# Performance work log

Hardware: AMD Instinct MI355X
Metric: run time of the kernel (lower is better)

Reference implementation:

```python
import jax, jax.numpy as jnp
import numpy as np

B, H, W, C = 32, 128, 128, 64
MX, MY = 32, 32  # modes_x, modes_y


def setup_inputs() -> dict:
    key = jax.random.key(0)
    k1, k2, k3, k4 = jax.random.split(key, 4)
    # glorot-ish scales for the spectral and conv weights
    wscale = (2.0 / (C + C)) ** 0.5
    return {
        "x": jax.random.normal(k1, (B, H, W, C), dtype=jnp.float32),
        "w_real": jax.random.normal(k2, (MX, MY, C, C), dtype=jnp.float32) * wscale,
        "w_imag": jax.random.normal(k3, (MX, MY, C, C), dtype=jnp.float32) * wscale,
        "conv_w": jax.random.normal(k4, (C, C), dtype=jnp.float32) * wscale,
        "conv_b": jnp.zeros((C,), dtype=jnp.float32),
    }


def reference(x, w_real, w_imag, conv_w, conv_b):
    # Complex spectral mixing weights [MX, MY, Cin, Cout]
    weights = jax.lax.complex(w_real, w_imag)
    # tf.signal.fft2d transforms the innermost TWO axes of [B,H,W,C],
    # i.e. axes (W, C); jnp.fft.fft2 default axes=(-2,-1) matches exactly.
    x_ft = jnp.fft.fft2(x.astype(jnp.complex64))           # [B,H,W,C] complex64
    # Mode truncation on axes (H, W), as in the original code.
    x_ft_trunc = x_ft[:, :MX, :MY, :]                      # [B,MX,MY,C]
    # Complex channel-mixing einsum over the low modes.
    x_ft_proc = jnp.einsum('bxyi,xyio->bxyo', x_ft_trunc, weights)  # [B,MX,MY,C]
    # Zero-pad back to the full grid on (H, W).
    x_ft_padded = jnp.pad(x_ft_proc,
                          ((0, 0), (0, H - MX), (0, W - MY), (0, 0)))
    # IFFT again over innermost two axes (W, C), take real part.
    x_spec = jnp.real(jnp.fft.ifft2(x_ft_padded))          # [B,H,W,C] float32
    # 1x1 conv (pointwise channel mix) + bias on the raw input.
    x_local = jnp.einsum('bhwi,io->bhwo', x, conv_w) + conv_b
    return jax.nn.relu(x_spec + x_local)
```

## Files before the change

kernel.cpp:

```cpp
#include <hip/hip_runtime.h>

typedef __attribute__((ext_vector_type(8))) short short8;
typedef __attribute__((ext_vector_type(4))) short bf16x4;
typedef __attribute__((ext_vector_type(4))) float f32x4;
typedef unsigned short ushort_t;

#define MFMA(a, b, c) __builtin_amdgcn_mfma_f32_16x16x32_bf16((a), (b), (c), 0, 0, 0)

constexpr int NB = 32, NHt = 128, NWd = 128, NC = 64, MX = 32;
constexpr float TWO_PI = 6.28318530717958647692f;

constexpr size_t TAB_T1 = 0;
constexpr size_t TAB_T2 = 16384;
constexpr size_t TAB_T3 = 32768;
constexpr size_t TAB_T4 = 49152;
constexpr size_t XY_OFF = 65536;

__device__ inline ushort_t f2bf(float f) {
    union { float f; unsigned int u; } v; v.f = f;
    unsigned int r = v.u + 0x7FFFu + ((v.u >> 16) & 1u);
    return (ushort_t)(r >> 16);
}
__device__ inline int sxor(int row) { return ((row >> 3) & 3) << 4; }

__global__ __launch_bounds__(256) void k0_tables(ushort_t* __restrict__ tabs)
{
    int e = blockIdx.x * 256 + threadIdx.x;
    int tab = e >> 9, rem = e & 511;
    float re[8], im[8];
    if (tab == 0) {
        int mt = rem >> 8, ks = (rem >> 6) & 3, l = rem & 63;
        int uu = (l & 15) + 16 * mt, wb = (l >> 4) * 8 + 32 * ks;
        #pragma unroll
        for (int j = 0; j < 8; ++j) {
            float a = (float)((uu * (wb + j)) & 127) * (TWO_PI / 128.f);
            re[j] = cosf(a); im[j] = -sinf(a);
        }
    } else if (tab == 1) {
        int nt = rem >> 7, ks = (rem >> 6) & 1, l = rem & 63;
        int kk = (l & 15) + 16 * nt, cb2 = (l >> 4) * 8 + 32 * ks;
        #pragma unroll
        for (int j = 0; j < 8; ++j) {
            float a = (float)((kk * (cb2 + j)) & 63) * (TWO_PI / 64.f);
            re[j] = cosf(a); im[j] = -sinf(a);
        }
    } else if (tab == 2) {
        int nt = rem >> 7, ks = (rem >> 6) & 1, l = rem & 63;
        int cc = (l & 15) + 16 * nt, ob = (l >> 4) * 8 + 32 * ks;
        #pragma unroll
        for (int j = 0; j < 8; ++j) {
            float a = (float)(((ob + j) * cc) & 63) * (TWO_PI / 64.f);
            re[j] = cosf(a); im[j] = sinf(a);
        }
    } else {
        int mt = rem >> 6, l = rem & 63;
        int w = (l & 15) + 16 * mt, ub = (l >> 4) * 8;
        #pragma unroll
        for (int j = 0; j < 8; ++j) {
            float a = (float)((w * (ub + j)) & 127) * (TWO_PI / 128.f);
            re[j] = cosf(a) * 0.0001220703125f;
            im[j] = sinf(a) * 0.0001220703125f;
        }
    }
    ushort_t* dst = tabs + (size_t)e * 16;
    #pragma unroll
    for (int j = 0; j < 8; ++j) { dst[j] = f2bf(re[j]); dst[8 + j] = f2bf(im[j]); }
}

__global__ __launch_bounds__(512) void k1_fwd(
    const float* __restrict__ x, const char* __restrict__ tabs, ushort_t* __restrict__ XY)
{
    const int b = blockIdx.x, h = blockIdx.y;
    const int tid = threadIdx.x, lane = tid & 63, wv = tid >> 6;
    constexpr int SXT  = 0;
    constexpr int M1RE = 17408;
    constexpr int M1IM = 17408 + 4608;
    __shared__ __align__(16) char sm[26624];

    const float* xs = x + ((size_t)(b * NHt + h)) * (NWd * NC);
    #pragma unroll
    for (int i = 0; i < 4; ++i) {
        int idx = tid + 512 * i;
        int w = idx >> 4, c4 = (idx & 15) * 4;
        f32x4 v = *reinterpret_cast<const f32x4*>(xs + w * 64 + c4);
        #pragma unroll
        for (int j = 0; j < 4; ++j)
            *(ushort_t*)(sm + SXT + (c4 + j) * 272 + ((w * 2) ^ sxor(c4 + j))) = f2bf(v[j]);
    }
    __syncthreads();

    const int mt = wv >> 2, nt = wv & 3;
    f32x4 m1r = {0.f,0.f,0.f,0.f}, m1i = {0.f,0.f,0.f,0.f};
    const int cc = (lane & 15) + 16 * nt;
    #pragma unroll
    for (int ks = 0; ks < 4; ++ks) {
        short8 bfrag = *reinterpret_cast<const short8*>(
            sm + SXT + cc * 272 + (((lane >> 4) * 16 + 64 * ks) ^ sxor(cc)));
        const char* t1 = tabs + TAB_T1 + (((mt * 4 + ks) * 64 + lane) * 32);
        short8 are = *reinterpret_cast<const short8*>(t1);
        short8 aim = *reinterpret_cast<const short8*>(t1 + 16);
        m1r = MFMA(are, bfrag, m1r);
        m1i = MFMA(aim, bfrag, m1i);
    }
    #pragma unroll
    for (int r = 0; r < 4; ++r) {
        int u = (lane >> 4) * 4 + r + 16 * mt;
        int c = (lane & 15) + 16 * nt;
        *(ushort_t*)(sm + M1RE + u * 144 + c * 2) = f2bf(m1r[r]);
        *(ushort_t*)(sm + M1IM + u * 144 + c * 2) = f2bf(m1i[r]);
    }
    __syncthreads();

    f32x4 xP = {0.f,0.f,0.f,0.f}, xQ = {0.f,0.f,0.f,0.f}, xI = {0.f,0.f,0.f,0.f};
    #pragma unroll
    for (int ks = 0; ks < 2; ++ks) {
        short8 are = *reinterpret_cast<const short8*>(
            sm + M1RE + ((lane & 15) + 16 * mt) * 144 + (lane >> 4) * 16 + 64 * ks);
        short8 aim = *reinterpret_cast<const short8*>(
            sm + M1IM + ((lane & 15) + 16 * mt) * 144 + (lane >> 4) * 16 + 64 * ks);
        const char* t2 = tabs + TAB_T2 + (((nt * 2 + ks) * 64 + lane) * 32);
        short8 bre = *reinterpret_cast<const short8*>(t2);
        short8 bim = *reinterpret_cast<const short8*>(t2 + 16);
        xP = MFMA(are, bre, xP);
        xQ = MFMA(aim, bim, xQ);
        xI = MFMA(are, bim, xI);
        xI = MFMA(aim, bre, xI);
    }
    #pragma unroll
    for (int r = 0; r < 4; ++r) {
        int u = (lane >> 4) * 4 + r + 16 * mt;
        int k = (lane & 15) + 16 * nt;
        *(ushort_t*)(sm + SXT + 0    + u * 128 + k * 2) = f2bf(xP[r] - xQ[r]);
        *(ushort_t*)(sm + SXT + 4096 + u * 128 + k * 2) = f2bf(xI[r]);
    }
    __syncthreads();

    {
        int u = tid >> 4, comp = (tid >> 3) & 1, k8 = (tid & 7) * 8;
        short8 v = *reinterpret_cast<const short8*>(sm + SXT + comp * 4096 + u * 128 + k8 * 2);
        size_t hu = (size_t)(h * 32 + u);
        *reinterpret_cast<short8*>(XY + ((hu * 2 + comp) * 32 + b) * 64 + k8) = v;
    }
}

__global__ __launch_bounds__(256) void k2_mix(
    const float* __restrict__ wre, const float* __restrict__ wim, ushort_t* __restrict__ XY)
{
    const int h = blockIdx.x, u = blockIdx.y;
    const int tid = threadIdx.x, lane = tid & 63, wv = tid >> 6;
    constexpr int XRE = 0, XIM = 4608, WTR = 9216, WTI = 18432;
    __shared__ __align__(16) char sm[27648];
    const size_t hu = (size_t)(h * 32 + u);

    #pragma unroll
    for (int it = 0; it < 2; ++it) {
        int row = (tid >> 3) + 32 * it;
        int comp = row >> 5, bb = row & 31, k8 = (tid & 7) * 8;
        short8 v = *reinterpret_cast<const short8*>(XY + ((hu * 2 + comp) * 32 + bb) * 64 + k8);
        *reinterpret_cast<short8*>(sm + (comp ? XIM : XRE) + bb * 144 + k8 * 2) = v;
    }
    const float* wr = wre + hu * 4096;
    const float* wi = wim + hu * 4096;
    #pragma unroll
    for (int i = 0; i < 4; ++i) {
        int idx = tid + 256 * i;
        int k = idx >> 4, o4 = (idx & 15) * 4;
        f32x4 vr = __builtin_nontemporal_load(reinterpret_cast<const f32x4*>(wr + k * 64 + o4));
        f32x4 vi = __builtin_nontemporal_load(reinterpret_cast<const f32x4*>(wi + k * 64 + o4));
        #pragma unroll
        for (int j = 0; j < 4; ++j) {
            int o = o4 + j, koff = (k * 2) ^ sxor(o);
            *(ushort_t*)(sm + WTR + o * 144 + koff) = f2bf(vr[j]);
            *(ushort_t*)(sm + WTI + o * 144 + koff) = f2bf(vi[j]);
        }
    }
    __syncthreads();

    const int mt = wv >> 1;
    f32x4 yRe[2], yIm[2];
    #pragma unroll
    for (int half = 0; half < 2; ++half) {
        const int nt = (wv & 1) * 2 + half;
        const int oo = (lane & 15) + 16 * nt;
        f32x4 yP = {0.f,0.f,0.f,0.f}, yQ = {0.f,0.f,0.f,0.f}, yI = {0.f,0.f,0.f,0.f};
        #pragma unroll
        for (int ks = 0; ks < 2; ++ks) {
            int woff = ((lane >> 4) * 16 + 64 * ks) ^ sxor(oo);
            short8 are = *reinterpret_cast<const short8*>(
                sm + XRE + ((lane & 15) + 16 * mt) * 144 + (lane >> 4) * 16 + 64 * ks);
            short8 aim = *reinterpret_cast<const short8*>(
                sm + XIM + ((lane & 15) + 16 * mt) * 144 + (lane >> 4) * 16 + 64 * ks);
            short8 bre = *reinterpret_cast<const short8*>(sm + WTR + oo * 144 + woff);
            short8 bim = *reinterpret_cast<const short8*>(sm + WTI + oo * 144 + woff);
            yP = MFMA(are, bre, yP); yQ = MFMA(aim, bim, yQ);
            yI = MFMA(are, bim, yI); yI = MFMA(aim, bre, yI);
        }
        #pragma unroll
        for (int r = 0; r < 4; ++r) { yRe[half][r] = yP[r] - yQ[r]; yIm[half][r] = yI[r]; }
    }
    __syncthreads();

    #pragma unroll
    for (int half = 0; half < 2; ++half) {
        const int nt = (wv & 1) * 2 + half;
        #pragma unroll
        for (int r = 0; r < 4; ++r) {
            int bb = (lane >> 4) * 4 + r + 16 * mt;
            int o = (lane & 15) + 16 * nt;
            *(ushort_t*)(sm + 0    + bb * 128 + o * 2) = f2bf(yRe[half][r]);
            *(ushort_t*)(sm + 4096 + bb * 128 + o * 2) = f2bf(yIm[half][r]);
        }
    }
    __syncthreads();

    #pragma unroll
    for (int it = 0; it < 2; ++it) {
        int flat = tid + 256 * it;
        short8 v = *reinterpret_cast<const short8*>(sm + flat * 16);
        *reinterpret_cast<short8*>(XY + hu * 4096 + flat * 8) = v;
    }
}

__global__ __launch_bounds__(512, 4) void k3_inv(
    const float* __restrict__ x, const float* __restrict__ cw, const float* __restrict__ cb,
    const char* __restrict__ tabs, const ushort_t* __restrict__ XY, float* __restrict__ out)
{
    const int b = blockIdx.x, h = blockIdx.y;
    const int tid = threadIdx.x, lane = tid & 63, wv = tid >> 6;
    constexpr int ST_RE = 0, ST_IM = 5120;
    constexpr int XB   = 10240;
    constexpr int CWT  = 28672;
    constexpr int SCB  = 37888;
    constexpr int OUTB = 38144;
    constexpr int YRE  = 38144;
    constexpr int YIM  = 38144 + 4608;
    __shared__ __align__(16) char sm[72960];

    const float* xs = x + ((size_t)(b * NHt + h)) * (NWd * NC);
    f32x4 xv[4];
    #pragma unroll
    for (int i = 0; i < 4; ++i) {
        int idx = tid + 512 * i;
        int w = idx >> 4, c4 = (idx & 15) * 4;
        xv[i] = __builtin_nontemporal_load(reinterpret_cast<const f32x4*>(xs + w * 64 + c4));
    }
    short8 yv = {}, gre = {}, gim = {};
    if (h < MX) {
        int u = tid >> 4, comp = (tid >> 3) & 1, o8 = (tid & 7) * 8;
        size_t hu = (size_t)(h * 32 + u);
        yv = *reinterpret_cast<const short8*>(XY + ((hu * 2 + comp) * 32 + b) * 64 + o8);
        const char* t4 = tabs + TAB_T4 + ((wv * 64 + lane) * 32);
        gre = *reinterpret_cast<const short8*>(t4);
        gim = *reinterpret_cast<const short8*>(t4 + 16);
    }

    #pragma unroll
    for (int i = 0; i < 4; ++i) {
        int idx = tid + 512 * i;
        int w = idx >> 4, c4 = (idx & 15) * 4;
        bf16x4 pk = { (short)f2bf(xv[i][0]), (short)f2bf(xv[i][1]),
                      (short)f2bf(xv[i][2]), (short)f2bf(xv[i][3]) };
        *reinterpret_cast<bf16x4*>(sm + XB + w * 144 + c4 * 2) = pk;
    }
    #pragma unroll
    for (int i = 0; i < 2; ++i) {
        int ii = (tid >> 4) + 32 * i;
        #pragma unroll
        for (int j = 0; j < 4; ++j) {
            int o = (tid & 15) + 16 * j;
            *(ushort_t*)(sm + CWT + o * 144 + ii * 2) = f2bf(cw[ii * 64 + o]);
        }
    }
    if (tid < 64) ((float*)(sm + SCB))[tid] = cb[tid];

    if (h < MX) {
        {
            int u = tid >> 4, comp = (tid >> 3) & 1, o8 = (tid & 7) * 8;
            *reinterpret_cast<short8*>(sm + (comp ? YIM : YRE) + u * 144 + o8 * 2) = yv;
        }
        __syncthreads();
        const int mt = wv >> 2, nt = wv & 3;
        f32x4 sP = {0.f,0.f,0.f,0.f}, sQ = {0.f,0.f,0.f,0.f}, sI = {0.f,0.f,0.f,0.f};
        #pragma unroll
        for (int ks = 0; ks < 2; ++ks) {
            short8 are = *reinterpret_cast<const short8*>(
                sm + YRE + ((lane & 15) + 16 * mt) * 144 + (lane >> 4) * 16 + 64 * ks);
            short8 aim = *reinterpret_cast<const short8*>(
                sm + YIM + ((lane & 15) + 16 * mt) * 144 + (lane >> 4) * 16 + 64 * ks);
            const char* t3 = tabs + TAB_T3 + (((nt * 2 + ks) * 64 + lane) * 32);
            short8 bre = *reinterpret_cast<const short8*>(t3);
            short8 bim = *reinterpret_cast<const short8*>(t3 + 16);
            sP = MFMA(are, bre, sP); sQ = MFMA(aim, bim, sQ);
            sI = MFMA(are, bim, sI); sI = MFMA(aim, bre, sI);
        }
        #pragma unroll
        for (int r = 0; r < 4; ++r) {
            int u = (lane >> 4) * 4 + r + 16 * mt;
            int c = (lane & 15) + 16 * nt;
            *(ushort_t*)(sm + ST_RE + c * 80 + u * 2) = f2bf(sP[r] - sQ[r]);
            *(ushort_t*)(sm + ST_IM + c * 80 + u * 2) = f2bf(sI[r]);
        }
    }
    __syncthreads();

    #pragma unroll
    for (int nt = 0; nt < 4; ++nt) {
        f32x4 acc = {0.f,0.f,0.f,0.f};
        #pragma unroll
        for (int ks = 0; ks < 2; ++ks) {
            short8 ah = *reinterpret_cast<const short8*>(
                sm + XB + ((lane & 15) + 16 * wv) * 144 + (lane >> 4) * 16 + 64 * ks);
            short8 bw = *reinterpret_cast<const short8*>(
                sm + CWT + ((lane & 15) + 16 * nt) * 144 + (lane >> 4) * 16 + 64 * ks);
            acc = MFMA(ah, bw, acc);
        }
        f32x4 sp = {0.f,0.f,0.f,0.f}, sq = {0.f,0.f,0.f,0.f};
        if (h < MX) {
            short8 bre = *reinterpret_cast<const short8*>(
                sm + ST_RE + ((lane & 15) + 16 * nt) * 80 + (lane >> 4) * 16);
            short8 bim = *reinterpret_cast<const short8*>(
                sm + ST_IM + ((lane & 15) + 16 * nt) * 80 + (lane >> 4) * 16);
            sp = MFMA(gre, bre, sp);
            sq = MFMA(gim, bim, sq);
        }
        #pragma unroll
        for (int r = 0; r < 4; ++r) {
            int w = (lane >> 4) * 4 + r + 16 * wv;
            int c = (lane & 15) + 16 * nt;
            float v = acc[r] + ((const float*)(sm + SCB))[c];
            if (h < MX) v += sp[r] - sq[r];
            *(float*)(sm + OUTB + w * 272 + c * 4) = fmaxf(v, 0.0f);
        }
    }
    __syncthreads();

    float* orow = out + ((size_t)(b * NHt + h)) * (NWd * NC);
    #pragma unroll
    for (int i = 0; i < 4; ++i) {
        int flat = tid + 512 * i;
        int w = flat >> 4, c4 = (flat & 15) * 4;
        f32x4 v = *reinterpret_cast<const f32x4*>(sm + OUTB + w * 272 + c4 * 4);
        __builtin_nontemporal_store(v, reinterpret_cast<f32x4*>(orow + w * 64 + c4));
    }
}

extern "C" void kernel_launch(void* const* d_in, const int* in_sizes, int n_in,
                              void* d_out, int out_size, void* d_ws, size_t ws_size,
                              hipStream_t stream) {
    const float* x      = (const float*)d_in[0];
    const float* w_real = (const float*)d_in[1];
    const float* w_imag = (const float*)d_in[2];
    const float* conv_w = (const float*)d_in[3];
    const float* conv_b = (const float*)d_in[4];
    float* out = (float*)d_out;

    ushort_t* tabs = (ushort_t*)d_ws;
    ushort_t* XY   = (ushort_t*)((char*)d_ws + XY_OFF);

    k0_tables<<<8, 256, 0, stream>>>(tabs);
    k1_fwd<<<dim3(NB, MX), 512, 0, stream>>>(x, (const char*)d_ws, XY);
    k2_mix<<<dim3(MX, 32), 256, 0, stream>>>(w_real, w_imag, XY);
    k3_inv<<<dim3(NB, NHt), 512, 0, stream>>>(x, conv_w, conv_b,
                                              (const char*)d_ws, XY, out);
}
```

Baseline: 83.91 us.

## Split final kernel into conv-only rows and spectral rows kernels

```diff
diff --git a/kernel.cpp b/kernel.cpp
--- a/kernel.cpp
+++ b/kernel.cpp
@@ -221,7 +221,7 @@
     }
 }
 
-__global__ __launch_bounds__(512, 4) void k3_inv(
+__global__ __launch_bounds__(512, 4) void k3_spec(
     const float* __restrict__ x, const float* __restrict__ cw, const float* __restrict__ cb,
     const char* __restrict__ tabs, const ushort_t* __restrict__ XY, float* __restrict__ out)
 {
@@ -244,8 +244,8 @@
         int w = idx >> 4, c4 = (idx & 15) * 4;
         xv[i] = __builtin_nontemporal_load(reinterpret_cast<const f32x4*>(xs + w * 64 + c4));
     }
-    short8 yv = {}, gre = {}, gim = {};
-    if (h < MX) {
+    short8 yv, gre, gim;
+    {
         int u = tid >> 4, comp = (tid >> 3) & 1, o8 = (tid & 7) * 8;
         size_t hu = (size_t)(h * 32 + u);
         yv = *reinterpret_cast<const short8*>(XY + ((hu * 2 + comp) * 32 + b) * 64 + o8);
@@ -272,13 +272,13 @@
         }
     }
     if (tid < 64) ((float*)(sm + SCB))[tid] = cb[tid];
-
-    if (h < MX) {
-        {
-            int u = tid >> 4, comp = (tid >> 3) & 1, o8 = (tid & 7) * 8;
-            *reinterpret_cast<short8*>(sm + (comp ? YIM : YRE) + u * 144 + o8 * 2) = yv;
-        }
-        __syncthreads();
+    {
+        int u = tid >> 4, comp = (tid >> 3) & 1, o8 = (tid & 7) * 8;
+        *reinterpret_cast<short8*>(sm + (comp ? YIM : YRE) + u * 144 + o8 * 2) = yv;
+    }
+    __syncthreads();
+
+    {
         const int mt = wv >> 2, nt = wv & 3;
         f32x4 sP = {0.f,0.f,0.f,0.f}, sQ = {0.f,0.f,0.f,0.f}, sI = {0.f,0.f,0.f,0.f};
         #pragma unroll
@@ -314,21 +314,90 @@
                 sm + CWT + ((lane & 15) + 16 * nt) * 144 + (lane >> 4) * 16 + 64 * ks);
             acc = MFMA(ah, bw, acc);
         }
+        short8 bre = *reinterpret_cast<const short8*>(
+            sm + ST_RE + ((lane & 15) + 16 * nt) * 80 + (lane >> 4) * 16);
+        short8 bim = *reinterpret_cast<const short8*>(
+            sm + ST_IM + ((lane & 15) + 16 * nt) * 80 + (lane >> 4) * 16);
         f32x4 sp = {0.f,0.f,0.f,0.f}, sq = {0.f,0.f,0.f,0.f};
-        if (h < MX) {
-            short8 bre = *reinterpret_cast<const short8*>(
-                sm + ST_RE + ((lane & 15) + 16 * nt) * 80 + (lane >> 4) * 16);
-            short8 bim = *reinterpret_cast<const short8*>(
-                sm + ST_IM + ((lane & 15) + 16 * nt) * 80 + (lane >> 4) * 16);
-            sp = MFMA(gre, bre, sp);
-            sq = MFMA(gim, bim, sq);
+        sp = MFMA(gre, bre, sp);
+        sq = MFMA(gim, bim, sq);
+        #pragma unroll
+        for (int r = 0; r < 4; ++r) {
+            int w = (lane >> 4) * 4 + r + 16 * wv;
+            int c = (lane & 15) + 16 * nt;
+            float v = acc[r] + ((const float*)(sm + SCB))[c] + sp[r] - sq[r];
+            *(float*)(sm + OUTB + w * 272 + c * 4) = fmaxf(v, 0.0f);
+        }
+    }
+    __syncthreads();
+
+    float* orow = out + ((size_t)(b * NHt + h)) * (NWd * NC);
+    #pragma unroll
+    for (int i = 0; i < 4; ++i) {
+        int flat = tid + 512 * i;
+        int w = flat >> 4, c4 = (flat & 15) * 4;
+        f32x4 v = *reinterpret_cast<const f32x4*>(sm + OUTB + w * 272 + c4 * 4);
+        __builtin_nontemporal_store(v, reinterpret_cast<f32x4*>(orow + w * 64 + c4));
+    }
+}
+
+__global__ __launch_bounds__(512, 6) void k3_conv(
+    const float* __restrict__ x, const float* __restrict__ cw, const float* __restrict__ cb,
+    float* __restrict__ out)
+{
+    const int b = blockIdx.x, h = blockIdx.y + MX;
+    const int tid = threadIdx.x, lane = tid & 63, wv = tid >> 6;
+    constexpr int CWT  = 0;
+    constexpr int SCB  = 9216;
+    constexpr int OUTB = 9472;
+    __shared__ __align__(16) char sm[44288];
+
+    const float* xs = x + ((size_t)(b * NHt + h)) * (NWd * NC);
+    const float* xrow = xs + (16 * wv + (lane & 15)) * 64 + (lane >> 4) * 8;
+    f32x4 xa[4];
+    #pragma unroll
+    for (int ks = 0; ks < 2; ++ks) {
+        xa[2*ks]   = __builtin_nontemporal_load(reinterpret_cast<const f32x4*>(xrow + 32 * ks));
+        xa[2*ks+1] = __builtin_nontemporal_load(reinterpret_cast<const f32x4*>(xrow + 32 * ks + 4));
+    }
+    #pragma unroll
+    for (int i = 0; i < 2; ++i) {
+        int ii = (tid >> 4) + 32 * i;
+        #pragma unroll
+        for (int j = 0; j < 4; ++j) {
+            int o = (tid & 15) + 16 * j;
+            *(ushort_t*)(sm + CWT + o * 144 + ii * 2) = f2bf(cw[ii * 64 + o]);
+        }
+    }
+    if (tid < 64) ((float*)(sm + SCB))[tid] = cb[tid];
+
+    short8 afr[2];
+    #pragma unroll
+    for (int ks = 0; ks < 2; ++ks) {
+        short8 t;
+        #pragma unroll
+        for (int j = 0; j < 4; ++j) {
+            t[j]     = (short)f2bf(xa[2*ks][j]);
+            t[4 + j] = (short)f2bf(xa[2*ks+1][j]);
+        }
+        afr[ks] = t;
+    }
+    __syncthreads();
+
+    #pragma unroll
+    for (int nt = 0; nt < 4; ++nt) {
+        f32x4 acc = {0.f,0.f,0.f,0.f};
+        #pragma unroll
+        for (int ks = 0; ks < 2; ++ks) {
+            short8 bw = *reinterpret_cast<const short8*>(
+                sm + CWT + ((lane & 15) + 16 * nt) * 144 + (lane >> 4) * 16 + 64 * ks);
+            acc = MFMA(afr[ks], bw, acc);
         }
         #pragma unroll
         for (int r = 0; r < 4; ++r) {
             int w = (lane >> 4) * 4 + r + 16 * wv;
             int c = (lane & 15) + 16 * nt;
             float v = acc[r] + ((const float*)(sm + SCB))[c];
-            if (h < MX) v += sp[r] - sq[r];
             *(float*)(sm + OUTB + w * 272 + c * 4) = fmaxf(v, 0.0f);
         }
     }
@@ -360,6 +429,7 @@
     k0_tables<<<8, 256, 0, stream>>>(tabs);
     k1_fwd<<<dim3(NB, MX), 512, 0, stream>>>(x, (const char*)d_ws, XY);
     k2_mix<<<dim3(MX, 32), 256, 0, stream>>>(w_real, w_imag, XY);
-    k3_inv<<<dim3(NB, NHt), 512, 0, stream>>>(x, conv_w, conv_b,
+    k3_conv<<<dim3(NB, NHt - MX), 512, 0, stream>>>(x, conv_w, conv_b, out);
+    k3_spec<<<dim3(NB, MX), 512, 0, stream>>>(x, conv_w, conv_b,
                                               (const char*)d_ws, XY, out);
 }
```

Result: slower. 87.24 us (+4.0%).
